# Optimization experiments

Measured on AMD Instinct MI355X. Metric: run time of the kernel, lower is better.

The kernel has to match this reference:

```python
import jax, jax.numpy as jnp
import numpy as np
import math

B, N, K, C_IN, C_OUT = 2, 16384, 16, 128, 128


def _gather_neighbors(x, idx):
    # x: [B, N, C], idx: [B, N, K] -> [B, N, K, C]
    return jax.vmap(lambda xb, ib: xb[ib])(x, idx)


def setup_inputs() -> dict:
    key = jax.random.key(0)
    k1, k2, k3 = jax.random.split(key, 3)
    x = jax.random.normal(k1, (B, N, C_IN), dtype=jnp.float32)
    edge_index = jax.random.randint(k2, (2, B, N, K), 0, N, dtype=jnp.int64)
    W = jax.random.normal(k3, (C_OUT, C_IN), dtype=jnp.float32) * (1.0 / math.sqrt(C_IN))
    b = jnp.zeros((C_OUT,), dtype=jnp.float32)
    return {"x": x, "edge_index": edge_index, "W": W, "b": b}


def reference(x, edge_index, W, b):
    # x: [B, N, C]; edge_index: [2, B, N, K]
    x_i = _gather_neighbors(x, edge_index[1])  # [B, N, K, C] (centers)
    x_j = _gather_neighbors(x, edge_index[0])  # [B, N, K, C] (neighbors)
    scale = 1.0 / math.sqrt(x_i.shape[-1])
    scores = jnp.einsum('bnkc,bnjc->bnkj', x_i, x_j) * scale  # [B, N, K, K]
    p_attn = jax.nn.softmax(scores, axis=-1)
    h_k = jnp.einsum('bnkj,bnjc->bnkc', p_attn, x_j).sum(axis=-2)  # [B, N, C]
    y = (x + h_k) @ W.T + b  # Linear(in_channels -> out_channels)
    return jax.nn.relu(y)
```

## Files before the change

kernel.cpp:

```cpp
#include <hip/hip_runtime.h>
#include <hip/hip_bf16.h>
#include <math.h>

#define BB 2
#define NN 16384
#define KK 16
#define CC 128
#define COUT 128
#define NODES (BB * NN)
#define SP 136
#define SQP 136
#define ZP 136
#define XBLK 2048

typedef __attribute__((ext_vector_type(8))) short bf16x8;
typedef __attribute__((ext_vector_type(4))) float f32x4;
typedef __attribute__((ext_vector_type(2))) float f32x2;

__device__ __forceinline__ bf16x8 cvt8(f32x4 a, f32x4 b) {
    union { bf16x8 v; __hip_bfloat162 h[4]; } u;
    u.h[0] = __float22bfloat162_rn(make_float2(a[0], a[1]));
    u.h[1] = __float22bfloat162_rn(make_float2(a[2], a[3]));
    u.h[2] = __float22bfloat162_rn(make_float2(b[0], b[1]));
    u.h[3] = __float22bfloat162_rn(make_float2(b[2], b[3]));
    return u.v;
}

template <int CTRL>
__device__ __forceinline__ float rot_add(float v) {
    int r = __builtin_amdgcn_update_dpp(0, __float_as_int(v), CTRL, 0xF, 0xF, true);
    return v + __int_as_float(r);
}
__device__ __forceinline__ float row16_sum(float v) {
    v = rot_add<0x128>(v); v = rot_add<0x124>(v);
    v = rot_add<0x122>(v); v = rot_add<0x121>(v);
    return v;
}
__device__ __forceinline__ float row16_sum4(float v) {
    v = rot_add<0x128>(v); v = rot_add<0x124>(v);
    return v;
}

__global__ __launch_bounds__(256) void cast_x(
    const float* __restrict__ x,
    __hip_bfloat16* __restrict__ xh,
    unsigned char* __restrict__ xq,
    const float* __restrict__ W,
    __hip_bfloat16* __restrict__ wh)
{
    const int bid = blockIdx.x;
    if (bid >= XBLK) {
        const int i = (bid - XBLK) * 256 + threadIdx.x;
        const f32x4* p = (const f32x4*)(W + (size_t)i * 8);
        f32x4 a = p[0];
        f32x4 b = p[1];
        *(bf16x8*)(wh + (size_t)i * 8) = cvt8(a, b);
        return;
    }
    const int i = bid * 256 + threadIdx.x;
    const f32x4* p = (const f32x4*)(x + (size_t)i * 8);
    f32x4 a = __builtin_nontemporal_load(p);
    f32x4 b = __builtin_nontemporal_load(p + 1);
    *(bf16x8*)(xh + (size_t)i * 8) = cvt8(a, b);
    int lo = __builtin_amdgcn_cvt_pk_fp8_f32(a[0], a[1], 0, false);
    lo     = __builtin_amdgcn_cvt_pk_fp8_f32(a[2], a[3], lo, true);
    int hi = __builtin_amdgcn_cvt_pk_fp8_f32(b[0], b[1], 0, false);
    hi     = __builtin_amdgcn_cvt_pk_fp8_f32(b[2], b[3], hi, true);
    int2 v; v.x = lo; v.y = hi;
    *(int2*)(xq + (size_t)i * 8) = v;
}

__device__ __forceinline__ float col_weight(f32x4 acc) {
    const float scale = 0.08838834764831843f;
    float w = 0.f;
    #pragma unroll
    for (int i = 0; i < 4; ++i) {
        float e = __expf(acc[i] * scale);
        float s = row16_sum(e);
        w += e * __builtin_amdgcn_rcpf(s);
    }
    w += __shfl_xor(w, 16, 64);
    w += __shfl_xor(w, 32, 64);
    return w;
}

__device__ __forceinline__ float2 reduce_h(const bf16x8* bfr, float wj,
                                           float* hb, int m, int q, int lane) {
    #pragma unroll
    for (int s = 0; s < 4; ++s) {
        union { bf16x8 v; unsigned short u[8]; } ub;
        ub.v = bfr[s];
        float f[8];
        #pragma unroll
        for (int e = 0; e < 8; ++e) {
            f[e] = __uint_as_float((unsigned)ub.u[e] << 16) * wj;
            f[e] = row16_sum4(f[e]);
        }
        if (m < 4) {
            f32x4 lo = {f[0], f[1], f[2], f[3]};
            f32x4 hi = {f[4], f[5], f[6], f[7]};
            *(f32x4*)&hb[m * 132 + 32 * s + 8 * q]     = lo;
            *(f32x4*)&hb[m * 132 + 32 * s + 8 * q + 4] = hi;
        }
    }
    float hx = 0.f, hy = 0.f;
    #pragma unroll
    for (int r = 0; r < 4; ++r) {
        float2 v = *(const float2*)&hb[r * 132 + 2 * lane];
        hx += v.x; hy += v.y;
    }
    return make_float2(hx, hy);
}

struct Rows { int2 q[4]; bf16x8 j[4]; };

__device__ __forceinline__ void gather_rows(
    int ejv, int eiv, int r, int c,
    const __hip_bfloat16* __restrict__ xbh,
    const unsigned char* __restrict__ xbq,
    Rows& g)
{
    #pragma unroll
    for (int gg = 0; gg < 4; ++gg) {
        int ri = __shfl(eiv, gg * 4 + r, 16);
        g.q[gg] = *(const int2*)(xbq + (size_t)ri * CC + c * 8);
    }
    #pragma unroll
    for (int gg = 0; gg < 4; ++gg) {
        int rj = __shfl(ejv, gg * 4 + r, 16);
        g.j[gg] = *(const bf16x8*)(xbh + (size_t)rj * CC + c * 8);
    }
}

__global__ __launch_bounds__(256, 5) void attn_fused(
    const __hip_bfloat16* __restrict__ xh,
    const unsigned char* __restrict__ xq,
    const int* __restrict__ edge,
    const __hip_bfloat16* __restrict__ wh,
    const float* __restrict__ bias,
    float* __restrict__ out)
{
    __shared__ __hip_bfloat16 stgj[4][16 * SP];
    __shared__ alignas(16) unsigned char stgq[4][16 * SQP];
    __shared__ __hip_bfloat16 zt[16][ZP];

    const int t = threadIdx.x;
    const int wv = t >> 6;
    const int lane = t & 63;
    const int m = lane & 15;
    const int q = lane >> 4;
    const int r = lane >> 4;
    const int c = lane & 15;
    const int base = blockIdx.x * 16;
    const int node0 = base + wv * 4;
    const int b = node0 >> 14;

    const __hip_bfloat16* xbh = xh + (size_t)b * (size_t)(NN * CC);
    const unsigned char*  xbq = xq + (size_t)b * (size_t)(NN * CC);
    __hip_bfloat16* sj = &stgj[wv][0];
    unsigned char*  sq = &stgq[wv][0];
    float*          hb = (float*)sq;

    int ejv[4], eiv[4];
    __hip_bfloat162 rxv[4];
    #pragma unroll
    for (int n = 0; n < 4; ++n) {
        const int* ej = edge + (size_t)(node0 + n) * KK;
        ejv[n] = __builtin_nontemporal_load(ej + m);
        eiv[n] = __builtin_nontemporal_load(ej + (size_t)NODES * KK + m);
        const int nloc = (node0 + n) & (NN - 1);
        rxv[n] = *(const __hip_bfloat162*)(xbh + (size_t)nloc * CC + 2 * lane);
    }

    Rows cur, nxt;
    gather_rows(ejv[0], eiv[0], r, c, xbh, xbq, cur);

    #pragma unroll
    for (int it = 0; it < 4; ++it) {
        #pragma unroll
        for (int g = 0; g < 4; ++g)
            *(int2*)(sq + (g * 4 + r) * SQP + c * 8) = cur.q[g];
        #pragma unroll
        for (int g = 0; g < 4; ++g)
            *(bf16x8*)(sj + (g * 4 + r) * SP + c * 8) = cur.j[g];

        if (it < 3)
            gather_rows(ejv[it + 1], eiv[it + 1], r, c, xbh, xbq, nxt);

        bf16x8 bfr[4];
        f32x4 acc = {0.f, 0.f, 0.f, 0.f};
        #pragma unroll
        for (int s = 0; s < 4; ++s) {
            int2 wb = *(const int2*)(sq + m * SQP + s * 32 + q * 8);
            bfr[s] = *(const bf16x8*)(sj + m * SP + s * 32 + q * 8);
            f32x2 f0 = __builtin_amdgcn_cvt_pk_f32_fp8(wb.x, false);
            f32x2 f1 = __builtin_amdgcn_cvt_pk_f32_fp8(wb.x, true);
            f32x2 f2 = __builtin_amdgcn_cvt_pk_f32_fp8(wb.y, false);
            f32x2 f3 = __builtin_amdgcn_cvt_pk_f32_fp8(wb.y, true);
            union { bf16x8 v; __hip_bfloat162 h[4]; } u;
            u.h[0] = __float22bfloat162_rn(make_float2(f0[0], f0[1]));
            u.h[1] = __float22bfloat162_rn(make_float2(f1[0], f1[1]));
            u.h[2] = __float22bfloat162_rn(make_float2(f2[0], f2[1]));
            u.h[3] = __float22bfloat162_rn(make_float2(f3[0], f3[1]));
            acc = __builtin_amdgcn_mfma_f32_16x16x32_bf16(u.v, bfr[s], acc, 0, 0, 0);
        }

        const float wj = col_weight(acc);
        float2 h = reduce_h(bfr, wj, hb, m, q, lane);

        float2 xc = __bfloat1622float2(rxv[it]);
        const int row = wv * 4 + it;
        *(__hip_bfloat162*)(&zt[row][2 * lane]) =
            __float22bfloat162_rn(make_float2(xc.x + h.x, xc.y + h.y));

        if (it < 3) cur = nxt;
    }

    __syncthreads();

    bf16x8 zfr[4];
    #pragma unroll
    for (int s = 0; s < 4; ++s)
        zfr[s] = *(const bf16x8*)(&zt[m][s * 32 + q * 8]);

    #pragma unroll
    for (int half = 0; half < 2; ++half) {
        const int ct = wv * 2 + half;
        const __hip_bfloat16* wp = wh + (size_t)(ct * 16 + m) * CC + q * 8;
        bf16x8 wfr[4];
        #pragma unroll
        for (int s = 0; s < 4; ++s)
            wfr[s] = *(const bf16x8*)(wp + s * 32);
        const float bv = bias[ct * 16 + m];
        f32x4 acc = {0.f, 0.f, 0.f, 0.f};
        #pragma unroll
        for (int s = 0; s < 4; ++s)
            acc = __builtin_amdgcn_mfma_f32_16x16x32_bf16(zfr[s], wfr[s], acc, 0, 0, 0);
        float* op = out + (size_t)(base + q * 4) * COUT + ct * 16 + m;
        #pragma unroll
        for (int i = 0; i < 4; ++i)
            op[(size_t)i * COUT] = fmaxf(acc[i] + bv, 0.f);
    }
}

extern "C" void kernel_launch(void* const* d_in, const int* in_sizes, int n_in,
                              void* d_out, int out_size, void* d_ws, size_t ws_size,
                              hipStream_t stream) {
    const float* x    = (const float*)d_in[0];
    const int*   edge = (const int*)d_in[1];
    const float* W    = (const float*)d_in[2];
    const float* bias = (const float*)d_in[3];
    float* out = (float*)d_out;
    __hip_bfloat16* xh = (__hip_bfloat16*)d_ws;
    unsigned char*  xq = (unsigned char*)d_ws + 8 * 1024 * 1024;
    __hip_bfloat16* wh = (__hip_bfloat16*)((char*)d_ws + 12 * 1024 * 1024);

    cast_x<<<XBLK + (COUT * CC) / (256 * 8), 256, 0, stream>>>(x, xh, xq, W, wh);
    attn_fused<<<NODES / 16, 256, 0, stream>>>(xh, xq, edge, wh, bias, out);
}
```

Measured before the change: 108.1 us.

## Quantize gathered rows to per-row int8 with scales instead of bf16+fp8

Replaces the bf16 copy and fp8 copy of x with a single per-row symmetric 8-bit quantization (offset by 128) plus a per-row scale array. Both the center and neighbor gathers now fetch 8-bit rows, halving neighbor gather bytes, and the prep kernel writes less. The residual term now reads fp32 x directly. Dequantization adds integer unpack and FMA work per element, and the value path now uses 8-bit precision, which may raise numerical error.

After: 112.5 us. 1.04x slower.

```diff
diff --git a/kernel.cpp b/kernel.cpp
--- a/kernel.cpp
+++ b/kernel.cpp
@@ -8,14 +8,12 @@
 #define CC 128
 #define COUT 128
 #define NODES (BB * NN)
-#define SP 136
 #define SQP 136
 #define ZP 136
 #define XBLK 2048
 
 typedef __attribute__((ext_vector_type(8))) short bf16x8;
 typedef __attribute__((ext_vector_type(4))) float f32x4;
-typedef __attribute__((ext_vector_type(2))) float f32x2;
 
 __device__ __forceinline__ bf16x8 cvt8(f32x4 a, f32x4 b) {
     union { bf16x8 v; __hip_bfloat162 h[4]; } u;
@@ -26,11 +24,33 @@
     return u.v;
 }
 
+__device__ __forceinline__ bf16x8 upq(int2 w, float s, float mb) {
+    unsigned wx = (unsigned)w.x, wy = (unsigned)w.y;
+    float f[8];
+    #pragma unroll
+    for (int e = 0; e < 4; ++e)
+        f[e] = fmaf((float)((wx >> (8 * e)) & 255u), s, mb);
+    #pragma unroll
+    for (int e = 0; e < 4; ++e)
+        f[4 + e] = fmaf((float)((wy >> (8 * e)) & 255u), s, mb);
+    union { bf16x8 v; __hip_bfloat162 h[4]; } u;
+    u.h[0] = __float22bfloat162_rn(make_float2(f[0], f[1]));
+    u.h[1] = __float22bfloat162_rn(make_float2(f[2], f[3]));
+    u.h[2] = __float22bfloat162_rn(make_float2(f[4], f[5]));
+    u.h[3] = __float22bfloat162_rn(make_float2(f[6], f[7]));
+    return u.v;
+}
+
 template <int CTRL>
 __device__ __forceinline__ float rot_add(float v) {
     int r = __builtin_amdgcn_update_dpp(0, __float_as_int(v), CTRL, 0xF, 0xF, true);
     return v + __int_as_float(r);
 }
+template <int CTRL>
+__device__ __forceinline__ float rot_max(float v) {
+    int r = __builtin_amdgcn_update_dpp(0, __float_as_int(v), CTRL, 0xF, 0xF, true);
+    return fmaxf(v, __int_as_float(r));
+}
 __device__ __forceinline__ float row16_sum(float v) {
     v = rot_add<0x128>(v); v = rot_add<0x124>(v);
     v = rot_add<0x122>(v); v = rot_add<0x121>(v);
@@ -40,11 +60,16 @@
     v = rot_add<0x128>(v); v = rot_add<0x124>(v);
     return v;
 }
-
-__global__ __launch_bounds__(256) void cast_x(
+__device__ __forceinline__ float row16_max(float v) {
+    v = rot_max<0x128>(v); v = rot_max<0x124>(v);
+    v = rot_max<0x122>(v); v = rot_max<0x121>(v);
+    return v;
+}
+
+__global__ __launch_bounds__(256) void quant_x(
     const float* __restrict__ x,
-    __hip_bfloat16* __restrict__ xh,
-    unsigned char* __restrict__ xq,
+    unsigned char* __restrict__ xu,
+    float* __restrict__ inv,
     const float* __restrict__ W,
     __hip_bfloat16* __restrict__ wh)
 {
@@ -61,13 +86,21 @@
     const f32x4* p = (const f32x4*)(x + (size_t)i * 8);
     f32x4 a = __builtin_nontemporal_load(p);
     f32x4 b = __builtin_nontemporal_load(p + 1);
-    *(bf16x8*)(xh + (size_t)i * 8) = cvt8(a, b);
-    int lo = __builtin_amdgcn_cvt_pk_fp8_f32(a[0], a[1], 0, false);
-    lo     = __builtin_amdgcn_cvt_pk_fp8_f32(a[2], a[3], lo, true);
-    int hi = __builtin_amdgcn_cvt_pk_fp8_f32(b[0], b[1], 0, false);
-    hi     = __builtin_amdgcn_cvt_pk_fp8_f32(b[2], b[3], hi, true);
-    int2 v; v.x = lo; v.y = hi;
-    *(int2*)(xq + (size_t)i * 8) = v;
+    float am = fmaxf(fmaxf(fmaxf(fabsf(a[0]), fabsf(a[1])), fmaxf(fabsf(a[2]), fabsf(a[3]))),
+                     fmaxf(fmaxf(fabsf(b[0]), fabsf(b[1])), fmaxf(fabsf(b[2]), fabsf(b[3]))));
+    am = row16_max(am);
+    am = fmaxf(am, 1e-20f);
+    const float sc = 127.0f / am;
+    unsigned d0 = 0, d1 = 0;
+    #pragma unroll
+    for (int e = 0; e < 4; ++e)
+        d0 |= (unsigned)(__float2int_rn(a[e] * sc) + 128) << (8 * e);
+    #pragma unroll
+    for (int e = 0; e < 4; ++e)
+        d1 |= (unsigned)(__float2int_rn(b[e] * sc) + 128) << (8 * e);
+    int2 v; v.x = (int)d0; v.y = (int)d1;
+    *(int2*)(xu + (size_t)i * 8) = v;
+    if ((i & 15) == 0) inv[i >> 4] = am * (1.0f / 127.0f);
 }
 
 __device__ __forceinline__ float col_weight(f32x4 acc) {
@@ -112,36 +145,36 @@
     return make_float2(hx, hy);
 }
 
-struct Rows { int2 q[4]; bf16x8 j[4]; };
+struct Rows { int2 qi[4]; int2 qj[4]; };
 
 __device__ __forceinline__ void gather_rows(
     int ejv, int eiv, int r, int c,
-    const __hip_bfloat16* __restrict__ xbh,
-    const unsigned char* __restrict__ xbq,
+    const unsigned char* __restrict__ xbu,
     Rows& g)
 {
     #pragma unroll
     for (int gg = 0; gg < 4; ++gg) {
         int ri = __shfl(eiv, gg * 4 + r, 16);
-        g.q[gg] = *(const int2*)(xbq + (size_t)ri * CC + c * 8);
+        g.qi[gg] = *(const int2*)(xbu + (size_t)ri * CC + c * 8);
     }
     #pragma unroll
     for (int gg = 0; gg < 4; ++gg) {
         int rj = __shfl(ejv, gg * 4 + r, 16);
-        g.j[gg] = *(const bf16x8*)(xbh + (size_t)rj * CC + c * 8);
+        g.qj[gg] = *(const int2*)(xbu + (size_t)rj * CC + c * 8);
     }
 }
 
 __global__ __launch_bounds__(256, 5) void attn_fused(
-    const __hip_bfloat16* __restrict__ xh,
-    const unsigned char* __restrict__ xq,
+    const float* __restrict__ x,
+    const unsigned char* __restrict__ xu,
+    const float* __restrict__ inv,
     const int* __restrict__ edge,
     const __hip_bfloat16* __restrict__ wh,
     const float* __restrict__ bias,
     float* __restrict__ out)
 {
-    __shared__ __hip_bfloat16 stgj[4][16 * SP];
-    __shared__ alignas(16) unsigned char stgq[4][16 * SQP];
+    __shared__ alignas(16) unsigned char stga[4][16 * SQP];
+    __shared__ alignas(16) unsigned char stgb[4][16 * SQP];
     __shared__ __hip_bfloat16 zt[16][ZP];
 
     const int t = threadIdx.x;
@@ -155,63 +188,60 @@
     const int node0 = base + wv * 4;
     const int b = node0 >> 14;
 
-    const __hip_bfloat16* xbh = xh + (size_t)b * (size_t)(NN * CC);
-    const unsigned char*  xbq = xq + (size_t)b * (size_t)(NN * CC);
-    __hip_bfloat16* sj = &stgj[wv][0];
-    unsigned char*  sq = &stgq[wv][0];
-    float*          hb = (float*)sq;
+    const unsigned char* xbu = xu  + (size_t)b * (size_t)(NN * CC);
+    const float*         xbf = x   + (size_t)b * (size_t)(NN * CC);
+    const float*         invb = inv + (size_t)b * NN;
+    unsigned char* sa = &stga[wv][0];
+    unsigned char* sb = &stgb[wv][0];
+    float*         hb = (float*)sa;
 
     int ejv[4], eiv[4];
-    __hip_bfloat162 rxv[4];
+    float sJv[4], sIv[4];
+    float2 rxv[4];
     #pragma unroll
     for (int n = 0; n < 4; ++n) {
         const int* ej = edge + (size_t)(node0 + n) * KK;
         ejv[n] = __builtin_nontemporal_load(ej + m);
         eiv[n] = __builtin_nontemporal_load(ej + (size_t)NODES * KK + m);
+        sJv[n] = invb[ejv[n]];
+        sIv[n] = invb[eiv[n]];
         const int nloc = (node0 + n) & (NN - 1);
-        rxv[n] = *(const __hip_bfloat162*)(xbh + (size_t)nloc * CC + 2 * lane);
+        rxv[n] = *(const float2*)(xbf + (size_t)nloc * CC + 2 * lane);
     }
 
     Rows cur, nxt;
-    gather_rows(ejv[0], eiv[0], r, c, xbh, xbq, cur);
+    gather_rows(ejv[0], eiv[0], r, c, xbu, cur);
 
     #pragma unroll
     for (int it = 0; it < 4; ++it) {
         #pragma unroll
         for (int g = 0; g < 4; ++g)
-            *(int2*)(sq + (g * 4 + r) * SQP + c * 8) = cur.q[g];
+            *(int2*)(sa + (g * 4 + r) * SQP + c * 8) = cur.qi[g];
         #pragma unroll
         for (int g = 0; g < 4; ++g)
-            *(bf16x8*)(sj + (g * 4 + r) * SP + c * 8) = cur.j[g];
+            *(int2*)(sb + (g * 4 + r) * SQP + c * 8) = cur.qj[g];
 
         if (it < 3)
-            gather_rows(ejv[it + 1], eiv[it + 1], r, c, xbh, xbq, nxt);
-
+            gather_rows(ejv[it + 1], eiv[it + 1], r, c, xbu, nxt);
+
+        const float sA = sIv[it], mA = -128.f * sA;
+        const float sB = sJv[it], mB = -128.f * sB;
         bf16x8 bfr[4];
         f32x4 acc = {0.f, 0.f, 0.f, 0.f};
         #pragma unroll
         for (int s = 0; s < 4; ++s) {
-            int2 wb = *(const int2*)(sq + m * SQP + s * 32 + q * 8);
-            bfr[s] = *(const bf16x8*)(sj + m * SP + s * 32 + q * 8);
-            f32x2 f0 = __builtin_amdgcn_cvt_pk_f32_fp8(wb.x, false);
-            f32x2 f1 = __builtin_amdgcn_cvt_pk_f32_fp8(wb.x, true);
-            f32x2 f2 = __builtin_amdgcn_cvt_pk_f32_fp8(wb.y, false);
-            f32x2 f3 = __builtin_amdgcn_cvt_pk_f32_fp8(wb.y, true);
-            union { bf16x8 v; __hip_bfloat162 h[4]; } u;
-            u.h[0] = __float22bfloat162_rn(make_float2(f0[0], f0[1]));
-            u.h[1] = __float22bfloat162_rn(make_float2(f1[0], f1[1]));
-            u.h[2] = __float22bfloat162_rn(make_float2(f2[0], f2[1]));
-            u.h[3] = __float22bfloat162_rn(make_float2(f3[0], f3[1]));
-            acc = __builtin_amdgcn_mfma_f32_16x16x32_bf16(u.v, bfr[s], acc, 0, 0, 0);
+            int2 wa = *(const int2*)(sa + m * SQP + s * 32 + q * 8);
+            int2 wb = *(const int2*)(sb + m * SQP + s * 32 + q * 8);
+            bfr[s] = upq(wb, sB, mB);
+            acc = __builtin_amdgcn_mfma_f32_16x16x32_bf16(upq(wa, sA, mA), bfr[s], acc, 0, 0, 0);
         }
 
         const float wj = col_weight(acc);
         float2 h = reduce_h(bfr, wj, hb, m, q, lane);
 
-        float2 xc = __bfloat1622float2(rxv[it]);
         const int row = wv * 4 + it;
         *(__hip_bfloat162*)(&zt[row][2 * lane]) =
-            __float22bfloat162_rn(make_float2(xc.x + h.x, xc.y + h.y));
+            __float22bfloat162_rn(make_float2(rxv[it].x + h.x, rxv[it].y + h.y));
 
         if (it < 3) cur = nxt;
     }
@@ -251,10 +281,10 @@
     const float* W    = (const float*)d_in[2];
     const float* bias = (const float*)d_in[3];
     float* out = (float*)d_out;
-    __hip_bfloat16* xh = (__hip_bfloat16*)d_ws;
-    unsigned char*  xq = (unsigned char*)d_ws + 8 * 1024 * 1024;
-    __hip_bfloat16* wh = (__hip_bfloat16*)((char*)d_ws + 12 * 1024 * 1024);
-
-    cast_x<<<XBLK + (COUT * CC) / (256 * 8), 256, 0, stream>>>(x, xh, xq, W, wh);
-    attn_fused<<<NODES / 16, 256, 0, stream>>>(xh, xq, edge, wh, bias, out);
-}
+    unsigned char*  xu  = (unsigned char*)d_ws;
+    float*          inv = (float*)((char*)d_ws + 4 * 1024 * 1024);
+    __hip_bfloat16* wh  = (__hip_bfloat16*)((char*)d_ws + 4 * 1024 * 1024 + 128 * 1024);
+
+    quant_x<<<XBLK + (COUT * CC) / (256 * 8), 256, 0, stream>>>(x, xu, inv, W, wh);
+    attn_fused<<<NODES / 16, 256, 0, stream>>>(x, xu, inv, edge, wh, bias, out);
+}
```
